# Performance work log

Hardware: AMD Instinct MI355X
Metric: run time of the kernel (lower is better)

Reference implementation:

```python
import jax, jax.numpy as jnp
import numpy as np

H = 8  # num_heads (hidden_size=512 -> head dim 64)

def setup_inputs() -> dict:
    key = jax.random.key(0)
    ks = jax.random.split(key, 14)
    B, D, N, S, L = 16, 512, 128, 14, 12
    f = lambda k, shp: jax.random.normal(k, shp, dtype=jnp.float32)
    return {
        "q": f(ks[0], (B, D, N, S)),
        "k": f(ks[1], (B, D, N, S)),
        "v": f(ks[2], (B, D, N, S)),
        "attn_bias": f(ks[3], (B, L, N, N, H)),
        "Wq": f(ks[4], (D, D)) * 0.02, "bq": f(ks[5], (D,)) * 0.02,
        "Wk": f(ks[6], (D, D)) * 0.02, "bk": f(ks[7], (D,)) * 0.02,
        "Wv": f(ks[8], (D, D)) * 0.02, "bv": f(ks[9], (D,)) * 0.02,
        "Wd": f(ks[10], (S, L)) * 0.02, "bd": f(ks[11], (S,)) * 0.02,  # Dimension1: in_len->14
        "Wo": f(ks[12], (D, D)) * 0.02, "bo": f(ks[13], (D,)) * 0.02,
    }


def reference(q, k, v, attn_bias, Wq, bq, Wk, bk, Wv, bv, Wd, bd, Wo, bo):
    B, D, N, S = q.shape
    d = D // H
    scale = d ** -0.5
    # transpose(1,3): [B,D,N,S] -> [B,S,N,D]
    qt = jnp.transpose(q, (0, 3, 2, 1))
    kt = jnp.transpose(k, (0, 3, 2, 1))
    vt = jnp.transpose(v, (0, 3, 2, 1))
    # linear projections + split heads: [B,S,N,H,d] -> [B,S,H,N,d]
    qh = (qt @ Wq.T + bq).reshape(B, S, N, H, d).transpose(0, 1, 3, 2, 4) * scale
    kh = (kt @ Wk.T + bk).reshape(B, S, N, H, d).transpose(0, 1, 3, 2, 4)
    vh = (vt @ Wv.T + bv).reshape(B, S, N, H, d).transpose(0, 1, 3, 2, 4)
    # scores over node axis: [B,S,H,N,N]
    scores = jnp.einsum('bshnd,bshmd->bshnm', qh, kh)
    # bias: [B,L,N,N,H] -(Linear over L)-> [B,S,N,N,H] -> [B,S,H,N,N]
    bias = jnp.einsum('blnmh,sl->bsnmh', attn_bias, Wd) + bd[None, :, None, None, None]
    scores = scores + jnp.transpose(bias, (0, 1, 4, 2, 3))
    # NOTE: original uses softmax over dim=3 (the query/node-row axis) - kept faithful
    attn = jax.nn.softmax(scores, axis=3)
    out = jnp.einsum('bshnm,bshmd->bshnd', attn, vh)
    out = jnp.transpose(out, (0, 1, 3, 2, 4)).reshape(B, S, N, D)
    # output projection (dropout is identity at inference)
    return out @ Wo.T + bo
```

## Files before the change

kernel.cpp:

```cpp
#include <hip/hip_runtime.h>


typedef unsigned short u16;
typedef __bf16 bf16x8 __attribute__((ext_vector_type(8)));
typedef float f32x4 __attribute__((ext_vector_type(4)));

#define GLDS16(g, l) __builtin_amdgcn_global_load_lds( \
    (const __attribute__((address_space(1))) void*)(g), \
    (__attribute__((address_space(3))) void*)(l), 16, 0, 0)

__device__ __forceinline__ u16 f2bf(float f) {
  unsigned u = __float_as_uint(f);
  u += 0x7fffu + ((u >> 16) & 1u);
  return (u16)(u >> 16);
}
__device__ __forceinline__ float bf2f(u16 b) {
  return __uint_as_float(((unsigned)b) << 16);
}

__global__ __launch_bounds__(256) void wconv_kernel(const float* __restrict__ Wq, const float* __restrict__ Wk,
                                                    const float* __restrict__ Wv, const float* __restrict__ Wo,
                                                    u16* __restrict__ wbf) {
  int idx = (blockIdx.x * 256 + threadIdx.x) * 4;
  int m = idx >> 18;
  int r = idx & 262143;
  const float* src = (m == 0) ? Wq : (m == 1) ? Wk : (m == 2) ? Wv : Wo;
  float sc = (m == 0) ? 0.125f : 1.0f;
  float4 v = *(const float4*)&src[r];
  ushort4 o;
  o.x = f2bf(v.x * sc); o.y = f2bf(v.y * sc); o.z = f2bf(v.z * sc); o.w = f2bf(v.w * sc);
  *(ushort4*)&wbf[idx] = o;
}

__global__ __launch_bounds__(256) void transpose_kernel(const float* __restrict__ q, const float* __restrict__ k,
                                                        const float* __restrict__ v, u16* __restrict__ xT) {
  __shared__ u16 tile[64 * 76];
  const int nst = blockIdx.x;
  const int dt  = blockIdx.y;
  const int z   = blockIdx.z;
  const int which = z >> 4, b = z & 15;
  const float* src = (which == 0) ? q : (which == 1) ? k : v;
  u16* dst = xT + which * 14680064;
  const int t = threadIdx.x;
  const int c4 = t & 15, r0 = t >> 4;
#pragma unroll
  for (int it = 0; it < 4; ++it) {
    int r = r0 + it * 16;
    float4 f = *(const float4*)&src[(b * 512 + dt * 64 + r) * 1792 + nst * 64 + c4 * 4];
    ushort4 o; o.x = f2bf(f.x); o.y = f2bf(f.y); o.z = f2bf(f.z); o.w = f2bf(f.w);
    *(ushort4*)&tile[r * 76 + c4 * 4] = o;
  }
  __syncthreads();
  const int dq = t & 15, nr0 = t >> 4;
#pragma unroll
  for (int it = 0; it < 4; ++it) {
    int nr = nr0 + it * 16;
    unsigned c = nst * 64 + nr;
    unsigned n = c / 14u, sI = c - n * 14u;
    ushort4 o;
    o.x = tile[(dq * 4 + 0) * 76 + nr];
    o.y = tile[(dq * 4 + 1) * 76 + nr];
    o.z = tile[(dq * 4 + 2) * 76 + nr];
    o.w = tile[(dq * 4 + 3) * 76 + nr];
    *(ushort4*)&dst[(b * 1792 + sI * 128 + n) * 512 + dt * 64 + dq * 4] = o;
  }
}

__device__ __forceinline__ void gemm128(const u16* __restrict__ Ag, const u16* __restrict__ Bg,
                                        u16* sA, u16* sB, f32x4 acc[2][8]) {
  const int t = threadIdx.x;
  const int w = t >> 6, l = t & 63;
  const int lw = l >> 4, ll16 = l & 15;
  for (int kb = 0; kb < 8; ++kb) {
#pragma unroll
    for (int it = 0; it < 4; ++it) {
      int c = w * 64 + it * 256 + l;
      int row = (c >> 2) & 127;
      int g = ((c >> 9) << 2) | (c & 3);
      int go = row * 512 + kb * 64 + g * 8;
      GLDS16(Ag + go, sA + (w * 64 + it * 256) * 8);
      GLDS16(Bg + go, sB + (w * 64 + it * 256) * 8);
    }
    __syncthreads();
#pragma unroll
    for (int kk = 0; kk < 2; ++kk) {
      const int ko = (kk << 12) + lw * 8;
      bf16x8 a0 = *(const bf16x8*)&sA[ko + (w * 32 + ll16) * 32];
      bf16x8 a1 = *(const bf16x8*)&sA[ko + (w * 32 + 16 + ll16) * 32];
#pragma unroll
      for (int mt = 0; mt < 8; ++mt) {
        bf16x8 bb = *(const bf16x8*)&sB[ko + (mt * 16 + ll16) * 32];
        acc[0][mt] = __builtin_amdgcn_mfma_f32_16x16x32_bf16(a0, bb, acc[0][mt], 0, 0, 0);
        acc[1][mt] = __builtin_amdgcn_mfma_f32_16x16x32_bf16(a1, bb, acc[1][mt], 0, 0, 0);
      }
    }
    __syncthreads();
  }
}

__global__ __launch_bounds__(256) void proj_kernel(const u16* __restrict__ xT, const u16* __restrict__ wbf,
                                                   const float* __restrict__ bq, const float* __restrict__ bk,
                                                   const float* __restrict__ bv, u16* __restrict__ qh) {
  __shared__ u16 sA[8192], sB[8192];
  const unsigned u = blockIdx.x;
  const int xcd = u & 7, slot = u >> 3;
  const int bx = slot & 3;
  const int gidx = xcd * 84 + (slot >> 2);
  const int by = gidx % 14;
  const int z  = gidx / 14;
  const int p = z >> 4, b = z & 15;
  const u16* Ag = xT + p * 14680064 + b * 917504 + by * 65536;
  const u16* Bg = wbf + p * 262144 + bx * 65536;
  const float* bvec = (p == 0) ? bq : (p == 1) ? bk : bv;
  const float bscale = (p == 0) ? 0.125f : 1.0f;
  u16* outp = qh + p * 14680064;

  f32x4 acc[2][8];
#pragma unroll
  for (int i = 0; i < 2; ++i)
#pragma unroll
    for (int j = 0; j < 8; ++j)
#pragma unroll
      for (int e = 0; e < 4; ++e) acc[i][j][e] = 0.f;

  gemm128(Ag, Bg, sA, sB, acc);

  const int t = threadIdx.x, w = t >> 6, l = t & 63;
  const int lw = l >> 4, ll16 = l & 15;
#pragma unroll
  for (int mt = 0; mt < 8; ++mt) {
    int e = bx * 128 + mt * 16 + ll16;
    float bias = bvec[e] * bscale;
    int hh = e >> 6, dd = e & 63;
#pragma unroll
    for (int nt = 0; nt < 2; ++nt) {
#pragma unroll
      for (int j = 0; j < 4; ++j) {
        int n = w * 32 + nt * 16 + lw * 4 + j;
        outp[(((b * 14 + by) * 8 + hh) << 13) + n * 64 + dd] = f2bf(acc[nt][mt][j] + bias);
      }
    }
  }
}

__global__ __launch_bounds__(256) void bias_kernel(const float* __restrict__ ab, const float* __restrict__ Wd,
                                                   const float* __restrict__ bd, u16* __restrict__ bias2) {
  __shared__ float abt[12 * 1056];
  const int n = blockIdx.x;
  const int b = blockIdx.y;
  const int t = threadIdx.x;
#pragma unroll
  for (int it = 0; it < 12; ++it) {
    int i = t + 256 * it;
    int lI = i >> 8, rem = i & 255;
    int m = rem >> 1, hq = rem & 1;
    float4 f = *(const float4*)&ab[(((b * 12 + lI) * 128 + n) * 128 + m) * 8 + hq * 4];
    float* dstp = &abt[lI * 1056 + (hq * 4) * 132 + m];
    dstp[0] = f.x; dstp[132] = f.y; dstp[264] = f.z; dstp[396] = f.w;
  }
  __syncthreads();
  const int h = t >> 5, m0 = (t & 31) * 4;
  float4 f4[12];
#pragma unroll
  for (int lI = 0; lI < 12; ++lI) f4[lI] = *(const float4*)&abt[lI * 1056 + h * 132 + m0];
  u16* outb = bias2 + (b * 128 + n) * 14336 + h * 128 + m0;
#pragma unroll
  for (int sI = 0; sI < 14; ++sI) {
    float r0 = bd[sI], r1 = bd[sI], r2 = bd[sI], r3 = bd[sI];
#pragma unroll
    for (int lI = 0; lI < 12; ++lI) {
      float wv = Wd[sI * 12 + lI];
      r0 += wv * f4[lI].x; r1 += wv * f4[lI].y; r2 += wv * f4[lI].z; r3 += wv * f4[lI].w;
    }
    ushort4 o; o.x = f2bf(r0); o.y = f2bf(r1); o.z = f2bf(r2); o.w = f2bf(r3);
    *(ushort4*)&outb[sI * 1024] = o;
  }
}

__global__ __launch_bounds__(256) void attn_kernel(const u16* __restrict__ qh, const u16* __restrict__ kh,
                                                   const u16* __restrict__ vh, const u16* __restrict__ bias2,
                                                   u16* __restrict__ attn_out) {
  __shared__ u16 smem[25600];
  u16* sBias = smem;
  u16* sQ = smem;
  u16* sK = smem + 8192;
  u16* sP = smem;
  u16* sOut = smem;
  u16* sV = smem + 17408;

  const int sI = blockIdx.x, h = blockIdx.y, b = blockIdx.z;
  const int t = threadIdx.x, w = t >> 6, l = t & 63;
  const int lw = l >> 4, ll16 = l & 15;
  const int bsh = ((b * 14 + sI) * 8 + h) << 13;

#pragma unroll
  for (int it = 0; it < 4; ++it) {
    int m = (t >> 3) + 32 * it;
    int dd0 = (t & 7) * 8;
    uint4 uu = *(const uint4*)&vh[bsh + m * 64 + dd0];
    const u16* pu = (const u16*)&uu;
    int mo = (m >> 3) * 512 + (m & 7);
#pragma unroll
    for (int j = 0; j < 8; ++j) {
      int d = dd0 + j;
      sV[mo + (d >> 4) * 128 + (d & 15) * 8] = pu[j];
    }
  }
  {
    const u16* bb = bias2 + (b * 128) * 14336 + sI * 1024 + h * 128;
#pragma unroll
    for (int it = 0; it < 8; ++it) {
      int c = t + 256 * it;
      int n = c >> 4, mc = c & 15;
      uint4 uu = *(const uint4*)&bb[n * 14336 + mc * 8];
      *(uint4*)&sBias[n * 136 + mc * 8] = uu;
    }
  }
  __syncthreads();

  f32x4 acc[8][2];
  const int mb = w * 32;
#pragma unroll
  for (int nt = 0; nt < 8; ++nt)
#pragma unroll
    for (int mtl = 0; mtl < 2; ++mtl)
#pragma unroll
      for (int j = 0; j < 4; ++j)
        acc[nt][mtl][j] = bf2f(sBias[(nt * 16 + lw * 4 + j) * 136 + mb + mtl * 16 + ll16]);
  __syncthreads();

#pragma unroll
  for (int it = 0; it < 4; ++it) {
    int c = w * 64 + it * 256 + l;
    int row = (c >> 2) & 127;
    int g = ((c >> 9) << 2) | (c & 3);
    int go = row * 64 + g * 8;
    GLDS16(qh + bsh + go, sQ + (w * 64 + it * 256) * 8);
    GLDS16(kh + bsh + go, sK + (w * 64 + it * 256) * 8);
  }
  __syncthreads();

#pragma unroll
  for (int ks = 0; ks < 2; ++ks) {
    const int ko = (ks << 12) + lw * 8;
    bf16x8 b0 = *(const bf16x8*)&sK[ko + (mb + ll16) * 32];
    bf16x8 b1 = *(const bf16x8*)&sK[ko + (mb + 16 + ll16) * 32];
#pragma unroll
    for (int nt = 0; nt < 8; ++nt) {
      bf16x8 a = *(const bf16x8*)&sQ[ko + (nt * 16 + ll16) * 32];
      acc[nt][0] = __builtin_amdgcn_mfma_f32_16x16x32_bf16(a, b0, acc[nt][0], 0, 0, 0);
      acc[nt][1] = __builtin_amdgcn_mfma_f32_16x16x32_bf16(a, b1, acc[nt][1], 0, 0, 0);
    }
  }

  float inv[2];
#pragma unroll
  for (int mtl = 0; mtl < 2; ++mtl) {
    float mx = -3.0e38f;
#pragma unroll
    for (int nt = 0; nt < 8; ++nt)
#pragma unroll
      for (int j = 0; j < 4; ++j) mx = fmaxf(mx, acc[nt][mtl][j]);
    mx = fmaxf(mx, __shfl_xor(mx, 16));
    mx = fmaxf(mx, __shfl_xor(mx, 32));
    float sum = 0.f;
#pragma unroll
    for (int nt = 0; nt < 8; ++nt)
#pragma unroll
      for (int j = 0; j < 4; ++j) {
        float e = __expf(acc[nt][mtl][j] - mx);
        acc[nt][mtl][j] = e;
        sum += e;
      }
    sum += __shfl_xor(sum, 16);
    sum += __shfl_xor(sum, 32);
    inv[mtl] = 1.0f / sum;
  }
  __syncthreads();

#pragma unroll
  for (int nt = 0; nt < 8; ++nt)
#pragma unroll
    for (int mtl = 0; mtl < 2; ++mtl)
#pragma unroll
      for (int j = 0; j < 4; ++j)
        sP[(w << 12) + (nt * 16 + lw * 4 + j) * 32 + mtl * 16 + ll16] = f2bf(acc[nt][mtl][j] * inv[mtl]);
  __syncthreads();

  f32x4 o[2][4];
#pragma unroll
  for (int i = 0; i < 2; ++i)
#pragma unroll
    for (int dt2 = 0; dt2 < 4; ++dt2)
#pragma unroll
      for (int e = 0; e < 4; ++e) o[i][dt2][e] = 0.f;
#pragma unroll
  for (int ks = 0; ks < 4; ++ks) {
    const int ko = (ks << 12) + lw * 8;
    bf16x8 a0 = *(const bf16x8*)&sP[ko + ((w * 2 + 0) * 16 + ll16) * 32];
    bf16x8 a1 = *(const bf16x8*)&sP[ko + ((w * 2 + 1) * 16 + ll16) * 32];
#pragma unroll
    for (int dt2 = 0; dt2 < 4; ++dt2) {
      bf16x8 bv2 = *(const bf16x8*)&sV[(ks * 4 + lw) * 512 + dt2 * 128 + ll16 * 8];
      o[0][dt2] = __builtin_amdgcn_mfma_f32_16x16x32_bf16(a0, bv2, o[0][dt2], 0, 0, 0);
      o[1][dt2] = __builtin_amdgcn_mfma_f32_16x16x32_bf16(a1, bv2, o[1][dt2], 0, 0, 0);
    }
  }
  __syncthreads();

#pragma unroll
  for (int t2 = 0; t2 < 2; ++t2)
#pragma unroll
    for (int dt2 = 0; dt2 < 4; ++dt2)
#pragma unroll
      for (int j = 0; j < 4; ++j) {
        int rn = w * 32 + t2 * 16 + lw * 4 + j;
        sOut[rn * 72 + dt2 * 16 + ll16] = f2bf(o[t2][dt2][j]);
      }
  __syncthreads();
  const int ob = ((b * 14 + sI) * 128) * 512 + h * 64;
#pragma unroll
  for (int i = 0; i < 4; ++i) {
    int c = t + 256 * i;
    int row = c >> 3, ch = c & 7;
    uint4 uu = *(const uint4*)&sOut[row * 72 + ch * 8];
    *(uint4*)&attn_out[ob + row * 512 + ch * 8] = uu;
  }
}

__global__ __launch_bounds__(256) void out_kernel(const u16* __restrict__ attn_out, const u16* __restrict__ wobf,
                                                  const float* __restrict__ bo, float* __restrict__ out) {
  __shared__ u16 sA[8192], sB[8192];
  const unsigned u = blockIdx.x;
  const int xcd = u & 7, slot = u >> 3;
  const int bx = slot & 3;
  const int by = xcd * 28 + (slot >> 2);
  f32x4 acc[2][8];
#pragma unroll
  for (int i = 0; i < 2; ++i)
#pragma unroll
    for (int j = 0; j < 8; ++j)
#pragma unroll
      for (int e = 0; e < 4; ++e) acc[i][j][e] = 0.f;

  gemm128(attn_out + by * 65536, wobf + bx * 65536, sA, sB, acc);

  const int t = threadIdx.x, w = t >> 6, l = t & 63;
  const int lw = l >> 4, ll16 = l & 15;
#pragma unroll
  for (int mt = 0; mt < 8; ++mt) {
    int e = bx * 128 + mt * 16 + ll16;
    float bias = bo[e];
#pragma unroll
    for (int nt = 0; nt < 2; ++nt) {
#pragma unroll
      for (int j = 0; j < 4; ++j) {
        int row = by * 128 + w * 32 + nt * 16 + lw * 4 + j;
        out[row * 512 + e] = acc[nt][mt][j] + bias;
      }
    }
  }
}

extern "C" void kernel_launch(void* const* d_in, const int* in_sizes, int n_in,
                              void* d_out, int out_size, void* d_ws, size_t ws_size,
                              hipStream_t stream) {
  (void)in_sizes; (void)n_in; (void)out_size; (void)ws_size;
  const float* q  = (const float*)d_in[0];
  const float* k  = (const float*)d_in[1];
  const float* v  = (const float*)d_in[2];
  const float* ab = (const float*)d_in[3];
  const float* Wq = (const float*)d_in[4];
  const float* bq = (const float*)d_in[5];
  const float* Wk = (const float*)d_in[6];
  const float* bk = (const float*)d_in[7];
  const float* Wv = (const float*)d_in[8];
  const float* bv = (const float*)d_in[9];
  const float* Wd = (const float*)d_in[10];
  const float* bd = (const float*)d_in[11];
  const float* Wo = (const float*)d_in[12];
  const float* bo = (const float*)d_in[13];
  float* out = (float*)d_out;

  u16* ws = (u16*)d_ws;
  u16* xT      = ws;
  u16* qh      = ws + 44040192;
  u16* wbf     = ws + 88080384;
  u16* bias2   = ws;
  u16* attnout = ws + 29360128;

  wconv_kernel<<<dim3(1024), dim3(256), 0, stream>>>(Wq, Wk, Wv, Wo, wbf);
  transpose_kernel<<<dim3(28, 8, 48), dim3(256), 0, stream>>>(q, k, v, xT);
  proj_kernel<<<dim3(2688), dim3(256), 0, stream>>>(xT, wbf, bq, bk, bv, qh);
  bias_kernel<<<dim3(128, 16), dim3(256), 0, stream>>>(ab, Wd, bd, bias2);
  attn_kernel<<<dim3(14, 8, 16), dim3(256), 0, stream>>>(qh, qh + 14680064, qh + 29360128, bias2, attnout);
  out_kernel<<<dim3(896), dim3(256), 0, stream>>>(attnout, wbf + 786432, bo, out);
}
```

Measured before the change: 464.5 us.

## Double-buffer LDS tiles in projection and output GEMMs to overlap loads

```diff
diff --git a/kernel.cpp b/kernel.cpp
--- a/kernel.cpp
+++ b/kernel.cpp
@@ -66,42 +66,65 @@
   }
 }
 
-__device__ __forceinline__ void gemm128(const u16* __restrict__ Ag, const u16* __restrict__ Bg,
-                                        u16* sA, u16* sB, f32x4 acc[2][8]) {
+__device__ __forceinline__ void stageAB(const u16* __restrict__ Ag, const u16* __restrict__ Bg,
+                                        int kb, u16* sA, u16* sB, int w, int l) {
+#pragma unroll
+  for (int it = 0; it < 4; ++it) {
+    int c = w * 64 + it * 256 + l;
+    int row = (c >> 2) & 127;
+    int g = ((c >> 9) << 2) | (c & 3);
+    int go = row * 512 + kb * 64 + g * 8;
+    GLDS16(Ag + go, sA + (w * 64 + it * 256) * 8);
+    GLDS16(Bg + go, sB + (w * 64 + it * 256) * 8);
+  }
+}
+
+__device__ __forceinline__ void mfma_step(const u16* sA, const u16* sB, f32x4 acc[2][8],
+                                          int w, int lw, int ll16) {
+#pragma unroll
+  for (int kk = 0; kk < 2; ++kk) {
+    const int ko = (kk << 12) + lw * 8;
+    bf16x8 a0 = *(const bf16x8*)&sA[ko + (w * 32 + ll16) * 32];
+    bf16x8 a1 = *(const bf16x8*)&sA[ko + (w * 32 + 16 + ll16) * 32];
+#pragma unroll
+    for (int mt = 0; mt < 8; ++mt) {
+      bf16x8 bb = *(const bf16x8*)&sB[ko + (mt * 16 + ll16) * 32];
+      acc[0][mt] = __builtin_amdgcn_mfma_f32_16x16x32_bf16(a0, bb, acc[0][mt], 0, 0, 0);
+      acc[1][mt] = __builtin_amdgcn_mfma_f32_16x16x32_bf16(a1, bb, acc[1][mt], 0, 0, 0);
+    }
+  }
+}
+
+__device__ __forceinline__ void gemm128_db(const u16* __restrict__ Ag, const u16* __restrict__ Bg,
+                                           u16* sm, f32x4 acc[2][8]) {
+  u16* sA0 = sm;            u16* sB0 = sm + 8192;
+  u16* sA1 = sm + 16384;    u16* sB1 = sm + 24576;
   const int t = threadIdx.x;
   const int w = t >> 6, l = t & 63;
   const int lw = l >> 4, ll16 = l & 15;
+
+  stageAB(Ag, Bg, 0, sA0, sB0, w, l);
+#pragma unroll
   for (int kb = 0; kb < 8; ++kb) {
-#pragma unroll
-    for (int it = 0; it < 4; ++it) {
-      int c = w * 64 + it * 256 + l;
-      int row = (c >> 2) & 127;
-      int g = ((c >> 9) << 2) | (c & 3);
-      int go = row * 512 + kb * 64 + g * 8;
-      GLDS16(Ag + go, sA + (w * 64 + it * 256) * 8);
-      GLDS16(Bg + go, sB + (w * 64 + it * 256) * 8);
-    }
-    __syncthreads();
-#pragma unroll
-    for (int kk = 0; kk < 2; ++kk) {
-      const int ko = (kk << 12) + lw * 8;
-      bf16x8 a0 = *(const bf16x8*)&sA[ko + (w * 32 + ll16) * 32];
-      bf16x8 a1 = *(const bf16x8*)&sA[ko + (w * 32 + 16 + ll16) * 32];
-#pragma unroll
-      for (int mt = 0; mt < 8; ++mt) {
-        bf16x8 bb = *(const bf16x8*)&sB[ko + (mt * 16 + ll16) * 32];
-        acc[0][mt] = __builtin_amdgcn_mfma_f32_16x16x32_bf16(a0, bb, acc[0][mt], 0, 0, 0);
-        acc[1][mt] = __builtin_amdgcn_mfma_f32_16x16x32_bf16(a1, bb, acc[1][mt], 0, 0, 0);
-      }
-    }
-    __syncthreads();
+    const u16* cA = (kb & 1) ? sA1 : sA0;
+    const u16* cB = (kb & 1) ? sB1 : sB0;
+    if (kb < 7) {
+      stageAB(Ag, Bg, kb + 1, (kb & 1) ? sA0 : sA1, (kb & 1) ? sB0 : sB1, w, l);
+      asm volatile("s_waitcnt vmcnt(8)" ::: "memory");
+    } else {
+      asm volatile("s_waitcnt vmcnt(0)" ::: "memory");
+    }
+    __builtin_amdgcn_s_barrier();
+    __builtin_amdgcn_sched_barrier(0);
+    mfma_step(cA, cB, acc, w, lw, ll16);
+    __builtin_amdgcn_s_barrier();
   }
 }
 
 __global__ __launch_bounds__(256) void proj_kernel(const u16* __restrict__ xT, const u16* __restrict__ wbf,
                                                    const float* __restrict__ bq, const float* __restrict__ bk,
                                                    const float* __restrict__ bv, u16* __restrict__ qh) {
-  __shared__ u16 sA[8192], sB[8192];
+  __shared__ u16 sm[32768];
   const unsigned u = blockIdx.x;
   const int xcd = u & 7, slot = u >> 3;
   const int bx = slot & 3;
@@ -123,7 +146,7 @@
 #pragma unroll
       for (int e = 0; e < 4; ++e) acc[i][j][e] = 0.f;
 
-  gemm128(Ag, Bg, sA, sB, acc);
+  gemm128_db(Ag, Bg, sm, acc);
 
   const int t = threadIdx.x, w = t >> 6, l = t & 63;
   const int lw = l >> 4, ll16 = l & 15;
@@ -330,7 +353,7 @@
 
 __global__ __launch_bounds__(256) void out_kernel(const u16* __restrict__ attn_out, const u16* __restrict__ wobf,
                                                   const float* __restrict__ bo, float* __restrict__ out) {
-  __shared__ u16 sA[8192], sB[8192];
+  __shared__ u16 sm[32768];
   const unsigned u = blockIdx.x;
   const int xcd = u & 7, slot = u >> 3;
   const int bx = slot & 3;
@@ -343,7 +366,7 @@
 #pragma unroll
       for (int e = 0; e < 4; ++e) acc[i][j][e] = 0.f;
 
-  gemm128(attn_out + by * 65536, wobf + bx * 65536, sA, sB, acc);
+  gemm128_db(attn_out + by * 65536, wobf + bx * 65536, sm, acc);
 
   const int t = threadIdx.x, w = t >> 6, l = t & 63;
   const int lw = l >> 4, ll16 = l & 15;
```

After: 458.0 us. Within noise of the previous version (-1.4%).
